# Performance work log

Hardware: AMD Instinct MI355X
Metric: run time of the kernel (lower is better)

Reference implementation:

```python
import jax, jax.numpy as jnp
import numpy as np

B, N_ENT, E, T, DEPTH, N_TREES = 512, 2000, 512, 512, 6, 2
N_LEAVES = 2 ** DEPTH  # 64


def setup_inputs() -> dict:
    key = jax.random.key(0)
    ks = jax.random.split(key, 20)
    s = lambda fan_in: 1.0 / np.sqrt(fan_in)
    inp = {
        "leaf_idx": jax.random.randint(ks[0], (B, N_TREES, N_LEAVES), 0, N_ENT),
        "ent_emb": jax.random.normal(ks[1], (N_ENT, E), jnp.float32),
        "th_emb": jax.random.normal(ks[2], (T,), jnp.float32),
        # two2one: Linear(2E,4E) ReLU Linear(4E,E) ReLU
        "w1": jax.random.normal(ks[3], (2 * E, 4 * E), jnp.float32) * s(2 * E),
        "b1": jnp.zeros((4 * E,), jnp.float32),
        "w2": jax.random.normal(ks[4], (4 * E, E), jnp.float32) * s(4 * E),
        "b2": jnp.zeros((E,), jnp.float32),
        # one2one: Linear(E,4E) ReLU Linear(4E,E) Tanh
        "o1": jax.random.normal(ks[5], (E, 4 * E), jnp.float32) * s(E),
        "ob1": jnp.zeros((4 * E,), jnp.float32),
        "o2": jax.random.normal(ks[6], (4 * E, E), jnp.float32) * s(4 * E),
        "ob2": jnp.zeros((E,), jnp.float32),
        # theorem head: (T + 2E) -> E -> E/2 -> E/4 -> 1
        "h1": jax.random.normal(ks[7], (T + N_TREES * E, E), jnp.float32) * s(T + N_TREES * E),
        "hb1": jnp.zeros((E,), jnp.float32),
        "h2": jax.random.normal(ks[8], (E, E // 2), jnp.float32) * s(E),
        "hb2": jnp.zeros((E // 2,), jnp.float32),
        "h3": jax.random.normal(ks[9], (E // 2, E // 4), jnp.float32) * s(E // 2),
        "hb3": jnp.zeros((E // 4,), jnp.float32),
        "h4": jax.random.normal(ks[10], (E // 4, 1), jnp.float32) * s(E // 4),
        "hb4": jnp.zeros((1,), jnp.float32),
    }
    return inp


def _two2one(x, w1, b1, w2, b2):
    # x: [..., n_pairs, 2E] -> [..., n_pairs, E]  (ReLU, ReLU)
    h = jax.nn.relu(x @ w1 + b1)
    return jax.nn.relu(h @ w2 + b2)


def _one2one(x, o1, ob1, o2, ob2):
    # ReLU then Tanh, as in one2one_layers
    h = jax.nn.relu(x @ o1 + ob1)
    return jnp.tanh(h @ o2 + ob2)


def reference(leaf_idx, ent_emb, th_emb, w1, b1, w2, b2, o1, ob1, o2, ob2,
              h1, hb1, h2, hb2, h3, hb3, h4, hb4):
    # Leaf embedding lookups: [B, N_TREES, N_LEAVES, E]
    x = ent_emb[leaf_idx]
    # Level-by-level binary tree reduction with the two2one MLP
    n = N_LEAVES
    while n > 1:
        x = x.reshape(B, N_TREES, n // 2, 2 * E)
        x = _two2one(x, w1, b1, w2, b2)
        n //= 2
    root = x.reshape(B, N_TREES, E)
    # Unary numerical function applied at each entity root (Tanh output)
    root = _one2one(root, o1, ob1, o2, ob2)
    # Theorem head: concat theorem embedding with the entity encodings
    feat = jnp.concatenate(
        [jnp.broadcast_to(th_emb, (B, T)), root.reshape(B, N_TREES * E)], axis=-1)
    z = jax.nn.relu(feat @ h1 + hb1)
    z = jax.nn.relu(z @ h2 + hb2)
    z = jax.nn.relu(z @ h3 + hb3)
    return jax.nn.sigmoid(z @ h4 + hb4)  # [B, 1]
```

## Files before the change

kernel.cpp:

```cpp
#include <hip/hip_runtime.h>
#include <cstddef>
#include <cstdint>


typedef _Float16 f16;
typedef _Float16 f16x8 __attribute__((ext_vector_type(8)));
typedef float f32x4 __attribute__((ext_vector_type(4)));

__device__ __forceinline__ void gll16(const void* g, void* l) {
  __builtin_amdgcn_global_load_lds(
      (const __attribute__((address_space(1))) void*)g,
      (__attribute__((address_space(3))) void*)l, 16, 0, 0);
}

#define BAR __builtin_amdgcn_s_barrier()
#define VM4 asm volatile("s_waitcnt vmcnt(4)" ::: "memory")
#define VM0 asm volatile("s_waitcnt vmcnt(0)" ::: "memory")

template <int GATHER>
__global__ __launch_bounds__(512, 1) void gemm256(
    const f16* __restrict__ A, const f16* __restrict__ Bt,
    const float* __restrict__ bias, f16* __restrict__ C, int N, int K,
    const int* __restrict__ lidx, const f16* __restrict__ entf) {
  __shared__ __align__(16) f16 As[2][2][128][64];
  __shared__ __align__(16) f16 Bs[2][2][128][64];
  const int tid = threadIdx.x;
  const int m0 = blockIdx.y * 256;
  const int n0 = blockIdx.x * 256;

  const int srow = tid >> 3;
  const int sk = ((tid & 7) ^ (srow & 7)) << 3;
  const f16* Asrc = GATHER ? (const f16*)nullptr
                           : (A + (size_t)(m0 + srow) * K + sk);
  const f16* Bsrc = Bt + (size_t)(n0 + srow) * K + sk;
  const int wvb = (tid >> 6) * 1024;

  int e0[2][2], e1[2][2];
  if (GATHER) {
#pragma unroll
    for (int h = 0; h < 2; ++h)
#pragma unroll
      for (int o = 0; o < 2; ++o) {
        const int grow = m0 + h * 128 + o * 64 + srow;
        e0[h][o] = lidx[2 * grow];
        e1[h][o] = lidx[2 * grow + 1];
      }
  }

#define SA(BUF, HALF, KB)                                               \
  {                                                                     \
    char* d_ = (char*)&As[BUF][HALF][0][0] + wvb;                       \
    if (!GATHER) {                                                      \
      const f16* s_ = Asrc + (size_t)((HALF)*128) * K + (KB);           \
      gll16(s_, d_);                                                    \
      gll16(s_ + (size_t)64 * K, d_ + 8192);                            \
    } else {                                                            \
      const int hs_ = (KB) >> 9;                                        \
      const int kk_ = ((KB)&511) + sk;                                  \
      const int ea_ = hs_ ? e1[HALF][0] : e0[HALF][0];                  \
      const int eb_ = hs_ ? e1[HALF][1] : e0[HALF][1];                  \
      gll16(entf + ((size_t)ea_ << 9) + kk_, d_);                       \
      gll16(entf + ((size_t)eb_ << 9) + kk_, d_ + 8192);                \
    }                                                                   \
  }
#define SB(BUF, HALF, KB)                                               \
  {                                                                     \
    char* d_ = (char*)&Bs[BUF][HALF][0][0] + wvb;                       \
    const f16* s_ = Bsrc + (size_t)((HALF)*128) * K + (KB);             \
    gll16(s_, d_);                                                      \
    gll16(s_ + (size_t)64 * K, d_ + 8192);                              \
  }

  const int l = tid & 63, wid = tid >> 6;
  const int wm = wid >> 2, wn = wid & 3;
  const int q = l & 15, kg = l >> 4;
  const int csw = (kg << 4) ^ ((q & 7) << 4);
  const char* Abase = (const char*)As + wm * 16384 + q * 128;
  const char* Bbase =
      (const char*)Bs + (wn >> 1) * 16384 + ((wn & 1) * 64 + q) * 128;

  f16x8 a[4], b[4][2];
  f32x4 acc[8][4] = {};

#define RD_B(BUF)                                                       \
  {                                                                     \
    _Pragma("unroll") for (int j_ = 0; j_ < 4; ++j_) {                  \
      b[j_][0] = *(const f16x8*)(Bbase + (BUF)*32768 + j_ * 2048 + csw);       \
      b[j_][1] = *(const f16x8*)(Bbase + (BUF)*32768 + j_ * 2048 + (csw ^ 64)); \
    }                                                                   \
  }
#define RD_A(BUF, HI, KS)                                               \
  {                                                                     \
    _Pragma("unroll") for (int i_ = 0; i_ < 4; ++i_)                    \
        a[i_] = *(const f16x8*)(Abase + (BUF)*32768 +                   \
                                ((HI)*4 + i_) * 2048 + (csw ^ ((KS) << 6))); \
  }
#define MM(HI, KS)                                                      \
  __builtin_amdgcn_s_setprio(1);                                        \
  {                                                                     \
    _Pragma("unroll") for (int i_ = 0; i_ < 4; ++i_) {                  \
      _Pragma("unroll") for (int j_ = 0; j_ < 4; ++j_) {                \
        acc[(HI)*4 + i_][j_] = __builtin_amdgcn_mfma_f32_16x16x32_f16(  \
            a[i_], b[j_][KS], acc[(HI)*4 + i_][j_], 0, 0, 0);           \
      }                                                                 \
    }                                                                   \
  }                                                                     \
  __builtin_amdgcn_s_setprio(0);

  SA(0, 0, 0); SA(0, 1, 0); SB(0, 0, 0); SB(0, 1, 0);
  SB(1, 0, 64); SB(1, 1, 64);
  VM4; BAR;

  const int niter = K >> 7;
  for (int it = 0; it < niter; ++it) {
    const int kt1 = (2 * it + 1) << 6;
    const int kt2 = (2 * it + 2) << 6;
    const int kt3 = (2 * it + 3) << 6;
    const bool pf = (it + 1) < niter;
    RD_B(0); RD_A(0, 0, 0); SA(1, 0, kt1);            BAR; MM(0, 0); BAR;
    RD_A(0, 1, 0); SA(1, 1, kt1);                     BAR; MM(1, 0); BAR;
    RD_A(0, 0, 1); if (pf) SB(0, 0, kt2);             BAR; MM(0, 1); BAR;
    RD_A(0, 1, 1); if (pf) SB(0, 1, kt2);
    if (pf) { VM4; } else { VM0; }                    BAR; MM(1, 1); BAR;
    RD_B(1); RD_A(1, 0, 0); if (pf) SA(0, 0, kt2);    BAR; MM(0, 0); BAR;
    RD_A(1, 1, 0); if (pf) SA(0, 1, kt2);             BAR; MM(1, 0); BAR;
    RD_A(1, 0, 1); if (pf) SB(1, 0, kt3);             BAR; MM(0, 1); BAR;
    RD_A(1, 1, 1); if (pf) { SB(1, 1, kt3); VM4; }    BAR; MM(1, 1); BAR;
  }
#undef SA
#undef SB
#undef RD_B
#undef RD_A
#undef MM

#pragma unroll
  for (int j = 0; j < 4; ++j) {
    const int col = n0 + wn * 64 + j * 16 + q;
    const float bsv = bias[col];
#pragma unroll
    for (int i = 0; i < 8; ++i) {
      f32x4 v = acc[i][j];
#pragma unroll
      for (int vi = 0; vi < 4; ++vi) {
        const int row = m0 + wm * 128 + i * 16 + kg * 4 + vi;
        C[(size_t)row * N + col] = (f16)fmaxf(v[vi] + bsv, 0.0f);
      }
    }
  }
}

template <int ACT, int OUTF32>
__global__ __launch_bounds__(256) void gemm128(
    const f16* __restrict__ A, const f16* __restrict__ Bt,
    const float* __restrict__ bias, void* __restrict__ Cout, int N, int K) {
  __shared__ __align__(16) f16 As[128 * 64];
  __shared__ __align__(16) f16 Bs[128 * 64];
  const int tid = threadIdx.x;
  const int m0 = blockIdx.y * 128;
  const int n0 = blockIdx.x * 128;
  const int srow = tid >> 3;
  const int sk = ((tid & 7) ^ ((tid >> 3) & 7)) << 3;
  const f16* Ag = A + (size_t)(m0 + srow) * K + sk;
  const f16* Bg = Bt + (size_t)(n0 + srow) * K + sk;
  char* Al = (char*)As + (tid >> 6) * 1024;
  char* Bl = (char*)Bs + (tid >> 6) * 1024;
  const int l = tid & 63;
  const int wm = tid >> 7;
  const int wn = (tid >> 6) & 1;
  const int q = l & 15;
  const int kg = l >> 4;
  const char* Ar = (const char*)As + (wm * 64 + q) * 128;
  const char* Br = (const char*)Bs + (wn * 64 + q) * 128;
  const int c0 = ((kg << 4) ^ ((q & 7) << 4));
  f32x4 acc[4][4] = {};
  for (int k0 = 0; k0 < K; k0 += 64) {
#pragma unroll
    for (int r = 0; r < 4; ++r) {
      gll16(Ag + (size_t)(r * 32) * K + k0, Al + r * 4096);
      gll16(Bg + (size_t)(r * 32) * K + k0, Bl + r * 4096);
    }
    __syncthreads();
#pragma unroll
    for (int ks = 0; ks < 2; ++ks) {
      const int cb = c0 ^ (ks << 6);
      f16x8 a[4], b[4];
#pragma unroll
      for (int i = 0; i < 4; ++i) a[i] = *(const f16x8*)(Ar + i * 2048 + cb);
#pragma unroll
      for (int j = 0; j < 4; ++j) b[j] = *(const f16x8*)(Br + j * 2048 + cb);
#pragma unroll
      for (int i = 0; i < 4; ++i)
#pragma unroll
        for (int j = 0; j < 4; ++j)
          acc[i][j] = __builtin_amdgcn_mfma_f32_16x16x32_f16(a[i], b[j],
                                                             acc[i][j], 0, 0, 0);
    }
    __syncthreads();
  }
#pragma unroll
  for (int j = 0; j < 4; ++j) {
    const int col = n0 + wn * 64 + j * 16 + q;
    const float bsv = bias[col];
#pragma unroll
    for (int i = 0; i < 4; ++i) {
      f32x4 v = acc[i][j];
#pragma unroll
      for (int vi = 0; vi < 4; ++vi) {
        const int row = m0 + wm * 64 + i * 16 + kg * 4 + vi;
        float c = v[vi] + bsv;
        if (ACT == 1) c = fmaxf(c, 0.0f);
        if (ACT == 2) c = tanhf(c);
        if (OUTF32)
          ((float*)Cout)[(size_t)row * N + col] = c;
        else
          ((f16*)Cout)[(size_t)row * N + col] = (f16)c;
      }
    }
  }
}

__global__ void transpose_cvt(const float* __restrict__ src,
                              f16* __restrict__ dst, int K, int N) {
  __shared__ f16 tile[32][33];
  const int k0 = blockIdx.x * 32, n0 = blockIdx.y * 32;
  const int tx = threadIdx.x & 31, ty = threadIdx.x >> 5;
  for (int r = ty; r < 32; r += 8)
    tile[r][tx] = (f16)src[(size_t)(k0 + r) * N + n0 + tx];
  __syncthreads();
  for (int r = ty; r < 32; r += 8)
    dst[(size_t)(n0 + r) * K + k0 + tx] = tile[tx][r];
}

__global__ void cvt_f16(const float* __restrict__ src, f16* __restrict__ dst) {
  const int g = blockIdx.x * 256 + threadIdx.x;
  const float4* s = (const float4*)(src + (size_t)g * 8);
  float4 v0 = s[0], v1 = s[1];
  f16x8 o;
  o[0] = (f16)v0.x; o[1] = (f16)v0.y; o[2] = (f16)v0.z; o[3] = (f16)v0.w;
  o[4] = (f16)v1.x; o[5] = (f16)v1.y; o[6] = (f16)v1.z; o[7] = (f16)v1.w;
  *(f16x8*)(dst + (size_t)g * 8) = o;
}

__global__ void build_feat_h(const float* __restrict__ th,
                             const f16* __restrict__ root,
                             f16* __restrict__ feat) {
  int idx = blockIdx.x * 256 + threadIdx.x;
  int b = idx / 1536;
  int c = idx - b * 1536;
  feat[idx] = (c < 512) ? (f16)th[c] : root[(size_t)b * 1024 + (c - 512)];
}

__global__ void head_final(const float* __restrict__ z3,
                           const float* __restrict__ h4,
                           const float* __restrict__ hb4,
                           float* __restrict__ out) {
  int row = blockIdx.x;
  int t = threadIdx.x;
  float v = z3[(size_t)row * 128 + t] * h4[t] +
            z3[(size_t)row * 128 + 64 + t] * h4[64 + t];
#pragma unroll
  for (int off = 32; off; off >>= 1) v += __shfl_down(v, off);
  if (t == 0) out[row] = 1.0f / (1.0f + expf(-(v + hb4[0])));
}

extern "C" void kernel_launch(void* const* d_in, const int* in_sizes, int n_in,
                              void* d_out, int out_size, void* d_ws,
                              size_t ws_size, hipStream_t stream) {
  const int* leaf_idx = (const int*)d_in[0];
  const float* ent_emb = (const float*)d_in[1];
  const float* th_emb = (const float*)d_in[2];
  const float* w1 = (const float*)d_in[3];
  const float* b1 = (const float*)d_in[4];
  const float* w2 = (const float*)d_in[5];
  const float* b2 = (const float*)d_in[6];
  const float* o1 = (const float*)d_in[7];
  const float* ob1 = (const float*)d_in[8];
  const float* o2 = (const float*)d_in[9];
  const float* ob2 = (const float*)d_in[10];
  const float* h1 = (const float*)d_in[11];
  const float* hb1 = (const float*)d_in[12];
  const float* h2 = (const float*)d_in[13];
  const float* hb2 = (const float*)d_in[14];
  const float* h3 = (const float*)d_in[15];
  const float* hb3 = (const float*)d_in[16];
  const float* h4 = (const float*)d_in[17];
  const float* hb4 = (const float*)d_in[18];
  float* out = (float*)d_out;

  char* p = (char*)d_ws;
  f16* w1t = (f16*)p;  p += (size_t)2048 * 1024 * 2;
  f16* w2t = (f16*)p;  p += (size_t)512 * 2048 * 2;
  f16* o1t = (f16*)p;  p += (size_t)2048 * 512 * 2;
  f16* o2t = (f16*)p;  p += (size_t)512 * 2048 * 2;
  f16* h1t = (f16*)p;  p += (size_t)512 * 1536 * 2;
  f16* h2t = (f16*)p;  p += (size_t)256 * 512 * 2;
  f16* h3t = (f16*)p;  p += (size_t)128 * 256 * 2;
  f16* entf = (f16*)p; p += (size_t)2000 * 512 * 2;
  f16* Hf   = (f16*)p; p += (size_t)32768 * 2048 * 2;
  f16* bufA = (f16*)p; p += (size_t)32768 * 512 * 2;
  f16* featf = (f16*)p; p += (size_t)512 * 1536 * 2;
  f16* z1h  = (f16*)p; p += (size_t)512 * 512 * 2;
  f16* z2h  = (f16*)p; p += (size_t)512 * 256 * 2;
  float* z3 = (float*)p; p += (size_t)512 * 128 * 4;
  f16* bufB = Hf + (size_t)32 * 1024 * 1024;

  transpose_cvt<<<dim3(1024 / 32, 2048 / 32), 256, 0, stream>>>(w1, w1t, 1024, 2048);
  transpose_cvt<<<dim3(2048 / 32, 512 / 32), 256, 0, stream>>>(w2, w2t, 2048, 512);
  transpose_cvt<<<dim3(512 / 32, 2048 / 32), 256, 0, stream>>>(o1, o1t, 512, 2048);
  transpose_cvt<<<dim3(2048 / 32, 512 / 32), 256, 0, stream>>>(o2, o2t, 2048, 512);
  transpose_cvt<<<dim3(1536 / 32, 512 / 32), 256, 0, stream>>>(h1, h1t, 1536, 512);
  transpose_cvt<<<dim3(512 / 32, 256 / 32), 256, 0, stream>>>(h2, h2t, 512, 256);
  transpose_cvt<<<dim3(256 / 32, 128 / 32), 256, 0, stream>>>(h3, h3t, 256, 128);
  cvt_f16<<<(2000 * 512) / 2048, 256, 0, stream>>>(ent_emb, entf);

  gemm256<1><<<dim3(8, 128), 512, 0, stream>>>(nullptr, w1t, b1, Hf, 2048,
                                               1024, leaf_idx, entf);
  gemm256<0><<<dim3(2, 128), 512, 0, stream>>>(Hf, w2t, b2, bufA, 512, 2048,
                                               nullptr, nullptr);
  gemm256<0><<<dim3(8, 64), 512, 0, stream>>>(bufA, w1t, b1, Hf, 2048, 1024,
                                              nullptr, nullptr);
  gemm128<1, 0><<<dim3(4, 128), 256, 0, stream>>>(Hf, w2t, b2, bufB, 512, 2048);
  gemm256<0><<<dim3(8, 32), 512, 0, stream>>>(bufB, w1t, b1, Hf, 2048, 1024,
                                              nullptr, nullptr);
  gemm128<1, 0><<<dim3(4, 64), 256, 0, stream>>>(Hf, w2t, b2, bufA, 512, 2048);
  gemm128<1, 0><<<dim3(16, 32), 256, 0, stream>>>(bufA, w1t, b1, Hf, 2048, 1024);
  gemm128<1, 0><<<dim3(4, 32), 256, 0, stream>>>(Hf, w2t, b2, bufB, 512, 2048);
  gemm128<1, 0><<<dim3(16, 16), 256, 0, stream>>>(bufB, w1t, b1, Hf, 2048, 1024);
  gemm128<1, 0><<<dim3(4, 16), 256, 0, stream>>>(Hf, w2t, b2, bufA, 512, 2048);
  gemm128<1, 0><<<dim3(16, 8), 256, 0, stream>>>(bufA, w1t, b1, Hf, 2048, 1024);
  gemm128<1, 0><<<dim3(4, 8), 256, 0, stream>>>(Hf, w2t, b2, bufB, 512, 2048);

  gemm128<1, 0><<<dim3(16, 8), 256, 0, stream>>>(bufB, o1t, ob1, Hf, 2048, 512);
  gemm128<2, 0><<<dim3(4, 8), 256, 0, stream>>>(Hf, o2t, ob2, bufA, 512, 2048);

  build_feat_h<<<(512 * 1536) / 256, 256, 0, stream>>>(th_emb, bufA, featf);
  gemm128<1, 0><<<dim3(4, 4), 256, 0, stream>>>(featf, h1t, hb1, z1h, 512, 1536);
  gemm128<1, 0><<<dim3(2, 4), 256, 0, stream>>>(z1h, h2t, hb2, z2h, 256, 512);
  gemm128<1, 1><<<dim3(1, 4), 256, 0, stream>>>(z2h, h3t, hb3, z3, 128, 256);
  head_final<<<512, 64, 0, stream>>>(z3, h4, hb4, out);
}
```

Baseline: 832.1 us.

## Replace 256x256 double-buffered GEMM with 256x128 triple-buffered pipeline

The big GEMM kernel switches from a 256x256 tile with two LDS buffers and eight-phase interleaving to a 256x128 tile with a three-stage LDS ring, prefetching two K-steps ahead. Each wave now computes a 64x64 sub-tile instead of 128x64, which cuts accumulator registers. The one-block-per-CU launch bound is dropped, so more blocks may co-reside. Grids double in the N dimension, which means more B reads and less reuse of the A tile per block, in exchange for deeper latency hiding and more parallelism.

```diff
diff --git a/kernel.cpp b/kernel.cpp
--- a/kernel.cpp
+++ b/kernel.cpp
@@ -14,19 +14,19 @@
 }
 
 #define BAR __builtin_amdgcn_s_barrier()
-#define VM4 asm volatile("s_waitcnt vmcnt(4)" ::: "memory")
+#define VM6 asm volatile("s_waitcnt vmcnt(6)" ::: "memory")
 #define VM0 asm volatile("s_waitcnt vmcnt(0)" ::: "memory")
 
 template <int GATHER>
-__global__ __launch_bounds__(512, 1) void gemm256(
+__global__ __launch_bounds__(512) void gemm_p(
     const f16* __restrict__ A, const f16* __restrict__ Bt,
     const float* __restrict__ bias, f16* __restrict__ C, int N, int K,
     const int* __restrict__ lidx, const f16* __restrict__ entf) {
-  __shared__ __align__(16) f16 As[2][2][128][64];
-  __shared__ __align__(16) f16 Bs[2][2][128][64];
+  __shared__ __align__(16) f16 As[3][256][64];
+  __shared__ __align__(16) f16 Bs[3][128][64];
   const int tid = threadIdx.x;
   const int m0 = blockIdx.y * 256;
-  const int n0 = blockIdx.x * 256;
+  const int n0 = blockIdx.x * 128;
 
   const int srow = tid >> 3;
   const int sk = ((tid & 7) ^ (srow & 7)) << 3;
@@ -35,102 +35,90 @@
   const f16* Bsrc = Bt + (size_t)(n0 + srow) * K + sk;
   const int wvb = (tid >> 6) * 1024;
 
-  int e0[2][2], e1[2][2];
+  int e0[4], e1[4];
   if (GATHER) {
 #pragma unroll
-    for (int h = 0; h < 2; ++h)
-#pragma unroll
-      for (int o = 0; o < 2; ++o) {
-        const int grow = m0 + h * 128 + o * 64 + srow;
-        e0[h][o] = lidx[2 * grow];
-        e1[h][o] = lidx[2 * grow + 1];
-      }
-  }
-
-#define SA(BUF, HALF, KB)                                               \
+    for (int r = 0; r < 4; ++r) {
+      const int grow = m0 + r * 64 + srow;
+      e0[r] = lidx[2 * grow];
+      e1[r] = lidx[2 * grow + 1];
+    }
+  }
+
+#define SA(S, R, KB)                                                    \
   {                                                                     \
-    char* d_ = (char*)&As[BUF][HALF][0][0] + wvb;                       \
+    char* d_ = (char*)As + (size_t)(S)*32768 + (R)*8192 + wvb;          \
     if (!GATHER) {                                                      \
-      const f16* s_ = Asrc + (size_t)((HALF)*128) * K + (KB);           \
-      gll16(s_, d_);                                                    \
-      gll16(s_ + (size_t)64 * K, d_ + 8192);                            \
+      gll16(Asrc + (size_t)((R)*64) * K + (KB), d_);                    \
     } else {                                                            \
-      const int hs_ = (KB) >> 9;                                        \
-      const int kk_ = ((KB)&511) + sk;                                  \
-      const int ea_ = hs_ ? e1[HALF][0] : e0[HALF][0];                  \
-      const int eb_ = hs_ ? e1[HALF][1] : e0[HALF][1];                  \
-      gll16(entf + ((size_t)ea_ << 9) + kk_, d_);                       \
-      gll16(entf + ((size_t)eb_ << 9) + kk_, d_ + 8192);                \
+      const int e_ = ((KB) >> 9) ? e1[R] : e0[R];                       \
+      gll16(entf + ((size_t)e_ << 9) + (((KB)&511) + sk), d_);          \
     }                                                                   \
   }
-#define SB(BUF, HALF, KB)                                               \
+#define SB(S, R, KB)                                                    \
   {                                                                     \
-    char* d_ = (char*)&Bs[BUF][HALF][0][0] + wvb;                       \
-    const f16* s_ = Bsrc + (size_t)((HALF)*128) * K + (KB);             \
-    gll16(s_, d_);                                                      \
-    gll16(s_ + (size_t)64 * K, d_ + 8192);                              \
+    char* d_ = (char*)Bs + (size_t)(S)*16384 + (R)*8192 + wvb;          \
+    gll16(Bsrc + (size_t)((R)*64) * K + (KB), d_);                      \
   }
 
   const int l = tid & 63, wid = tid >> 6;
-  const int wm = wid >> 2, wn = wid & 3;
+  const int wm = wid >> 1, wn = wid & 1;
   const int q = l & 15, kg = l >> 4;
   const int csw = (kg << 4) ^ ((q & 7) << 4);
-  const char* Abase = (const char*)As + wm * 16384 + q * 128;
-  const char* Bbase =
-      (const char*)Bs + (wn >> 1) * 16384 + ((wn & 1) * 64 + q) * 128;
-
-  f16x8 a[4], b[4][2];
-  f32x4 acc[8][4] = {};
-
-#define RD_B(BUF)                                                       \
-  {                                                                     \
-    _Pragma("unroll") for (int j_ = 0; j_ < 4; ++j_) {                  \
-      b[j_][0] = *(const f16x8*)(Bbase + (BUF)*32768 + j_ * 2048 + csw);       \
-      b[j_][1] = *(const f16x8*)(Bbase + (BUF)*32768 + j_ * 2048 + (csw ^ 64)); \
-    }                                                                   \
-  }
-#define RD_A(BUF, HI, KS)                                               \
+  const char* Abase = (const char*)As + (wm * 64 + q) * 128;
+  const char* Bbase = (const char*)Bs + (wn * 64 + q) * 128;
+
+  f16x8 a[4], b[4];
+  f32x4 acc[4][4] = {};
+
+#define RD(S, KS)                                                       \
   {                                                                     \
     _Pragma("unroll") for (int i_ = 0; i_ < 4; ++i_)                    \
-        a[i_] = *(const f16x8*)(Abase + (BUF)*32768 +                   \
-                                ((HI)*4 + i_) * 2048 + (csw ^ ((KS) << 6))); \
-  }
-#define MM(HI, KS)                                                      \
+        a[i_] = *(const f16x8*)(Abase + (S)*32768 + i_ * 2048 +         \
+                                (csw ^ ((KS) << 6)));                   \
+    _Pragma("unroll") for (int j_ = 0; j_ < 4; ++j_)                    \
+        b[j_] = *(const f16x8*)(Bbase + (S)*16384 + j_ * 2048 +         \
+                                (csw ^ ((KS) << 6)));                   \
+  }
+#define MM                                                              \
   __builtin_amdgcn_s_setprio(1);                                        \
   {                                                                     \
     _Pragma("unroll") for (int i_ = 0; i_ < 4; ++i_) {                  \
       _Pragma("unroll") for (int j_ = 0; j_ < 4; ++j_) {                \
-        acc[(HI)*4 + i_][j_] = __builtin_amdgcn_mfma_f32_16x16x32_f16(  \
-            a[i_], b[j_][KS], acc[(HI)*4 + i_][j_], 0, 0, 0);           \
+        acc[i_][j_] = __builtin_amdgcn_mfma_f32_16x16x32_f16(           \
+            a[i_], b[j_], acc[i_][j_], 0, 0, 0);                        \
       }                                                                 \
     }                                                                   \
   }                                                                     \
   __builtin_amdgcn_s_setprio(0);
 
-  SA(0, 0, 0); SA(0, 1, 0); SB(0, 0, 0); SB(0, 1, 0);
+  SA(0, 0, 0); SA(0, 1, 0); SA(0, 2, 0); SA(0, 3, 0); SB(0, 0, 0); SB(0, 1, 0);
+  SA(1, 0, 64); SA(1, 1, 64); SA(1, 2, 64); SA(1, 3, 64);
   SB(1, 0, 64); SB(1, 1, 64);
-  VM4; BAR;
-
-  const int niter = K >> 7;
-  for (int it = 0; it < niter; ++it) {
-    const int kt1 = (2 * it + 1) << 6;
-    const int kt2 = (2 * it + 2) << 6;
-    const int kt3 = (2 * it + 3) << 6;
-    const bool pf = (it + 1) < niter;
-    RD_B(0); RD_A(0, 0, 0); SA(1, 0, kt1);            BAR; MM(0, 0); BAR;
-    RD_A(0, 1, 0); SA(1, 1, kt1);                     BAR; MM(1, 0); BAR;
-    RD_A(0, 0, 1); if (pf) SB(0, 0, kt2);             BAR; MM(0, 1); BAR;
-    RD_A(0, 1, 1); if (pf) SB(0, 1, kt2);
-    if (pf) { VM4; } else { VM0; }                    BAR; MM(1, 1); BAR;
-    RD_B(1); RD_A(1, 0, 0); if (pf) SA(0, 0, kt2);    BAR; MM(0, 0); BAR;
-    RD_A(1, 1, 0); if (pf) SA(0, 1, kt2);             BAR; MM(1, 0); BAR;
-    RD_A(1, 0, 1); if (pf) SB(1, 0, kt3);             BAR; MM(0, 1); BAR;
-    RD_A(1, 1, 1); if (pf) { SB(1, 1, kt3); VM4; }    BAR; MM(1, 1); BAR;
+  VM6; BAR;
+
+  const int nt = K >> 6;
+  int s = 0;
+  for (int t = 0; t < nt; ++t) {
+    const int s2 = (s + 2 >= 3) ? (s - 1) : (s + 2);
+    const int kb2 = (t + 2) << 6;
+    const bool pf = (t + 2) < nt;
+    RD(s, 0);
+    if (pf) { SA(s2, 0, kb2); SA(s2, 1, kb2); SA(s2, 2, kb2); }
+    BAR; MM; BAR;
+    RD(s, 1);
+    if (pf) {
+      SA(s2, 3, kb2); SB(s2, 0, kb2); SB(s2, 1, kb2);
+      VM6;
+    } else {
+      VM0;
+    }
+    BAR; MM; BAR;
+    s = (s + 1 == 3) ? 0 : (s + 1);
   }
 #undef SA
 #undef SB
-#undef RD_B
-#undef RD_A
+#undef RD
 #undef MM
 
 #pragma unroll
@@ -138,11 +126,11 @@
     const int col = n0 + wn * 64 + j * 16 + q;
     const float bsv = bias[col];
 #pragma unroll
-    for (int i = 0; i < 8; ++i) {
+    for (int i = 0; i < 4; ++i) {
       f32x4 v = acc[i][j];
 #pragma unroll
       for (int vi = 0; vi < 4; ++vi) {
-        const int row = m0 + wm * 128 + i * 16 + kg * 4 + vi;
+        const int row = m0 + wm * 64 + i * 16 + kg * 4 + vi;
         C[(size_t)row * N + col] = (f16)fmaxf(v[vi] + bsv, 0.0f);
       }
     }
@@ -313,14 +301,14 @@
   transpose_cvt<<<dim3(256 / 32, 128 / 32), 256, 0, stream>>>(h3, h3t, 256, 128);
   cvt_f16<<<(2000 * 512) / 2048, 256, 0, stream>>>(ent_emb, entf);
 
-  gemm256<1><<<dim3(8, 128), 512, 0, stream>>>(nullptr, w1t, b1, Hf, 2048,
+  gemm_p<1><<<dim3(16, 128), 512, 0, stream>>>(nullptr, w1t, b1, Hf, 2048,
                                                1024, leaf_idx, entf);
-  gemm256<0><<<dim3(2, 128), 512, 0, stream>>>(Hf, w2t, b2, bufA, 512, 2048,
-                                               nullptr, nullptr);
-  gemm256<0><<<dim3(8, 64), 512, 0, stream>>>(bufA, w1t, b1, Hf, 2048, 1024,
+  gemm_p<0><<<dim3(4, 128), 512, 0, stream>>>(Hf, w2t, b2, bufA, 512, 2048,
+                                              nullptr, nullptr);
+  gemm_p<0><<<dim3(16, 64), 512, 0, stream>>>(bufA, w1t, b1, Hf, 2048, 1024,
                                               nullptr, nullptr);
   gemm128<1, 0><<<dim3(4, 128), 256, 0, stream>>>(Hf, w2t, b2, bufB, 512, 2048);
-  gemm256<0><<<dim3(8, 32), 512, 0, stream>>>(bufB, w1t, b1, Hf, 2048, 1024,
+  gemm_p<0><<<dim3(16, 32), 512, 0, stream>>>(bufB, w1t, b1, Hf, 2048, 1024,
                                               nullptr, nullptr);
   gemm128<1, 0><<<dim3(4, 64), 256, 0, stream>>>(Hf, w2t, b2, bufA, 512, 2048);
   gemm128<1, 0><<<dim3(16, 32), 256, 0, stream>>>(bufA, w1t, b1, Hf, 2048, 1024);
```

Result: slower. 874.6 us (+5.1%).
